# Kernel optimization log

Measured on AMD Instinct MI355X. Metric: run time of the kernel, lower is better.

Reference implementation:

```python
import jax, jax.numpy as jnp
import numpy as np

B, T, I = 32, 128, 512
H, L, O = 512, 2, 512


def _uniform(key, shape, std):
    return jax.random.uniform(key, shape, jnp.float32, -std, std)


def setup_inputs() -> dict:
    key = jax.random.key(0)
    ks = jax.random.split(key, 12)
    std = 1.0 / np.sqrt(H)
    inp = {
        "x": jax.random.normal(ks[0], (B, T, I), jnp.float32),
        # stacked params: [L, 2, ...]; dir 0 = forward cells, dir 1 = reverse cells
        "Wxh": _uniform(ks[1], (L, 2, I, 2 * H), std),
        "bxh": _uniform(ks[2], (L, 2, 2 * H), std),
        "Whh": _uniform(ks[3], (L, 2, H, 2 * H), std),
        "bhh": _uniform(ks[4], (L, 2, 2 * H), std),
        "Wxr": _uniform(ks[5], (L, 2, I, H), std),
        "bxr": _uniform(ks[6], (L, 2, H), std),
        "Whr": _uniform(ks[7], (L, 2, H, H), std),
        "bhr": _uniform(ks[8], (L, 2, H, ), std),
        "Wfc": _uniform(ks[9], (2 * H, O), 1.0 / np.sqrt(2 * H)),
        "bfc": _uniform(ks[10], (O,), 1.0 / np.sqrt(2 * H)),
    }
    return inp


def gru_layer(seq, Wxh_l, bxh_l, Whh_l, bhh_l, Wxr_l, bxr_l, Whr_l, bhr_l):
    # seq: [T, B, I]. Precompute input projections for all timesteps (one big GEMM),
    # then scan the sequential h-dependent part.
    xh = jnp.einsum('tbi,ih->tbh', seq, Wxh_l) + bxh_l  # [T,B,2H]
    xr = jnp.einsum('tbi,ih->tbh', seq, Wxr_l) + bxr_l  # [T,B,H]

    def step(h, inp):
        xh_t, xr_t = inp
        zr = xh_t + h @ Whh_l + bhh_l
        z, r = jnp.split(zr, 2, axis=-1)
        z = jax.nn.sigmoid(z)
        r = jax.nn.sigmoid(r)
        g = jnp.tanh((h @ Whr_l + bhr_l) * r + xr_t)
        h = z * h + (1.0 - z) * g
        return h, h

    h0 = jnp.zeros((seq.shape[1], Whh_l.shape[0]), seq.dtype)
    _, out = jax.lax.scan(step, h0, (xh, xr))
    return out  # [T,B,H]


def reference(x, Wxh, bxh, Whh, bhh, Wxr, bxr, Whr, bhr, Wfc, bfc):
    # Faithful translation of BidirRecurrentModel.forward (GRU mode):
    # forward stream scans time-ordered input; reverse stream independently scans
    # the time-reversed input (the two streams are NOT concatenated between layers).
    seq_f = jnp.transpose(x, (1, 0, 2))   # [T,B,I]
    seq_r = seq_f[::-1]                   # reversed time order
    n_layers = Wxh.shape[0]
    for l in range(n_layers):
        seq_f = gru_layer(seq_f, Wxh[l, 0], bxh[l, 0], Whh[l, 0], bhh[l, 0],
                          Wxr[l, 0], bxr[l, 0], Whr[l, 0], bhr[l, 0])
        seq_r = gru_layer(seq_r, Wxh[l, 1], bxh[l, 1], Whh[l, 1], bhh[l, 1],
                          Wxr[l, 1], bxr[l, 1], Whr[l, 1], bhr[l, 1])
    # out = last fwd timestep; out_rev = FIRST element of reverse-ordered stream
    # (i.e. the reverse cell's state after one step), exactly as in the source.
    out = jnp.concatenate([seq_f[-1], seq_r[0]], axis=1)  # [B, 2H]
    return out @ Wfc + bfc  # [B, O]
```

## Files before the change

### kernel.cpp

```cpp
#include <hip/hip_runtime.h>
#include <hip/hip_bf16.h>

#define PROJ_ELEMS 12582912
#define SEQ_ELEMS  4194304
#define SLAB_PER_BLK 6144

__global__ __launch_bounds__(256)
void proj_kernel(const float* __restrict__ src,
                 const float* __restrict__ Wxh, const float* __restrict__ bxh,
                 const float* __restrict__ Wxr, const float* __restrict__ bxr,
                 __hip_bfloat16* __restrict__ proj, int layer)
{
    __shared__ float As[32][137];
    __shared__ float Ws[32][132];
    const int tid  = threadIdx.x;
    const int col0 = blockIdx.x * 128;
    const int row0 = blockIdx.y * 128;
    const int d    = row0 >> 12;
    const int ld   = layer * 2 + d;
    const int tx = tid & 15, ty = tid >> 4;

    const bool is_xr = (col0 >= 1024);
    const float* Wbase = is_xr ? (Wxr + (size_t)ld * 512 * 512 + (col0 - 1024))
                               : (Wxh + (size_t)ld * 512 * 1024 + col0);
    const int wstride = is_xr ? 512 : 1024;
    const float* bias = is_xr ? (bxr + ld * 512 + (col0 - 1024))
                              : (bxh + ld * 1024 + col0);

    float acc[8][8];
    #pragma unroll
    for (int i = 0; i < 8; i++)
        #pragma unroll
        for (int j = 0; j < 8; j++) acc[i][j] = 0.f;

    for (int k0 = 0; k0 < 512; k0 += 32) {
        #pragma unroll
        for (int v = 0; v < 4; v++) {
            int idx = tid + v * 256;
            int r   = idx >> 3;
            int c4  = (idx & 7) << 2;
            int gm  = row0 + r;
            int rr  = gm & 4095;
            int tt  = rr >> 5, bb = rr & 31;
            const float* p;
            if (layer == 0) {
                int ts = (gm >= 4096) ? (127 - tt) : tt;
                p = src + ((size_t)bb * 128 + ts) * 512 + (k0 + c4);
            } else {
                p = src + (((size_t)(gm >> 12) * 128 + tt) * 32 + bb) * 512 + (k0 + c4);
            }
            float4 vv = *(const float4*)p;
            As[c4 + 0][r] = vv.x; As[c4 + 1][r] = vv.y;
            As[c4 + 2][r] = vv.z; As[c4 + 3][r] = vv.w;
        }
        #pragma unroll
        for (int v = 0; v < 4; v++) {
            int idx = tid + v * 256;
            int kr  = idx >> 5;
            int c4  = (idx & 31) << 2;
            *(float4*)&Ws[kr][c4] = *(const float4*)(Wbase + (size_t)(k0 + kr) * wstride + c4);
        }
        __syncthreads();
        #pragma unroll
        for (int kk = 0; kk < 32; kk++) {
            float a[8], w[8];
            *(float4*)&a[0] = *(const float4*)&As[kk][ty * 8];
            *(float4*)&a[4] = *(const float4*)&As[kk][ty * 8 + 4];
            *(float4*)&w[0] = *(const float4*)&Ws[kk][tx * 8];
            *(float4*)&w[4] = *(const float4*)&Ws[kk][tx * 8 + 4];
            #pragma unroll
            for (int i = 0; i < 8; i++)
                #pragma unroll
                for (int j = 0; j < 8; j++)
                    acc[i][j] += a[i] * w[j];
        }
        __syncthreads();
    }
    #pragma unroll
    for (int i = 0; i < 8; i++) {
        int gm = row0 + ty * 8 + i;
        __hip_bfloat16* dst = proj + (size_t)gm * 1536 + col0 + tx * 8;
        #pragma unroll
        for (int j = 0; j < 8; j++)
            dst[j] = __float2bfloat16(acc[i][j] + bias[tx * 8 + j]);
    }
}

__global__ __launch_bounds__(256)
void repack_kernel(const float* __restrict__ Whh, const float* __restrict__ Whr,
                   float* __restrict__ slabs)
{
    const int blk = blockIdx.x;
    const int ld = blk >> 7, jb = blk & 127;
    const float* WhhL = Whh + (size_t)ld * 512 * 1024;
    const float* WhrL = Whr + (size_t)ld * 512 * 512;
    float* out = slabs + (size_t)blk * SLAB_PER_BLK;
    for (int u = 0; u < 24; u++) {
        int idx = threadIdx.x + u * 256;
        int rec = idx / 12, r3 = idx % 12;
        int g = rec >> 2, cg = rec & 3;
        int e = r3 >> 2, ki = r3 & 3;
        int k = g * 4 + ki, j = jb * 4 + cg;
        float v;
        if (e == 0)      v = WhhL[(size_t)k * 1024 + j];
        else if (e == 1) v = WhhL[(size_t)k * 1024 + 512 + j];
        else             v = WhrL[(size_t)k * 512 + j];
        out[idx] = v;
    }
}

__global__ __launch_bounds__(256)
void step_kernel(const __hip_bfloat16* __restrict__ proj, float* __restrict__ seq,
                 const float* __restrict__ slabs,
                 const float* __restrict__ bhh, const float* __restrict__ bhr,
                 int layer, int t)
{
    __shared__ __align__(16) float hs[32 * 512];
    const int tid = threadIdx.x;
    const int d   = blockIdx.x >> 7;
    const int jb  = blockIdx.x & 127;
    const int ld  = layer * 2 + d;
    const int cg  = tid & 3;
    const int kh  = (tid >> 2) & 1;
    const int b   = tid >> 3;
    const int j   = jb * 4 + cg;
    const int sb  = b & 7;

    float az = 0.f, ar = 0.f, ag = 0.f;
    float hv_self = 0.f;

    if (t > 0) {
        const float* hsrc = seq + ((size_t)(d * 128 + (t - 1)) * 32) * 512;
        #pragma unroll
        for (int v = 0; v < 16; v++) {
            int id = tid + v * 256;
            int bb = id >> 7, g = id & 127;
            float4 hv = *(const float4*)(hsrc + (size_t)id * 4);
            *(float4*)&hs[bb * 512 + ((g ^ (bb & 7)) << 2)] = hv;
        }
        __syncthreads();

        const float4* wrec = (const float4*)slabs + (size_t)(ld * 128 + jb) * 1536;
        #pragma unroll 4
        for (int gg = 0; gg < 64; gg++) {
            int g = kh * 64 + gg;
            float4 h4 = *(const float4*)&hs[b * 512 + ((g ^ sb) << 2)];
            const float4* wp = wrec + (size_t)(g * 4 + cg) * 3;
            float4 wz = wp[0], wr = wp[1], wg = wp[2];
            az += h4.x * wz.x + h4.y * wz.y + h4.z * wz.z + h4.w * wz.w;
            ar += h4.x * wr.x + h4.y * wr.y + h4.z * wr.z + h4.w * wr.w;
            ag += h4.x * wg.x + h4.y * wg.y + h4.z * wg.z + h4.w * wg.w;
        }
        az += __shfl_xor(az, 4, 64);
        ar += __shfl_xor(ar, 4, 64);
        ag += __shfl_xor(ag, 4, 64);
        hv_self = hs[b * 512 + ((jb ^ sb) << 2) + cg];
    }

    const size_t pb = ((size_t)(d * 128 + t) * 32 + b) * 1536;
    float pz = __bfloat162float(proj[pb + j]);
    float pr = __bfloat162float(proj[pb + 512 + j]);
    float pg = __bfloat162float(proj[pb + 1024 + j]);
    float bz = bhh[ld * 1024 + j];
    float br = bhh[ld * 1024 + 512 + j];
    float bg = bhr[ld * 512 + j];
    float z  = 1.f / (1.f + __expf(-(az + pz + bz)));
    float r  = 1.f / (1.f + __expf(-(ar + pr + br)));
    float gt = tanhf((ag + bg) * r + pg);
    float hn = z * hv_self + (1.f - z) * gt;
    if (kh == 0)
        seq[((size_t)(d * 128 + t) * 32 + b) * 512 + j] = hn;
}

__global__ __launch_bounds__(256)
void fc_kernel(const float* __restrict__ seq, const float* __restrict__ Wfc,
               const float* __restrict__ bfc, float* __restrict__ out)
{
    int idx = blockIdx.x * 256 + threadIdx.x;
    int b = idx >> 9, o = idx & 511;
    const float* catf = seq + ((size_t)(0 * 128 + 127) * 32 + b) * 512;
    const float* catr = seq + ((size_t)(1 * 128 + 0) * 32 + b) * 512;
    float acc = bfc[o];
    #pragma unroll 8
    for (int k = 0; k < 512; k++) acc += catf[k] * Wfc[(size_t)k * 512 + o];
    #pragma unroll 8
    for (int k = 0; k < 512; k++) acc += catr[k] * Wfc[(size_t)(512 + k) * 512 + o];
    out[(size_t)b * 512 + o] = acc;
}

extern "C" void kernel_launch(void* const* d_in, const int* in_sizes, int n_in,
                              void* d_out, int out_size, void* d_ws, size_t ws_size,
                              hipStream_t stream) {
    (void)in_sizes; (void)n_in; (void)out_size; (void)ws_size;
    const float* x   = (const float*)d_in[0];
    const float* Wxh = (const float*)d_in[1];
    const float* bxh = (const float*)d_in[2];
    const float* Whh = (const float*)d_in[3];
    const float* bhh = (const float*)d_in[4];
    const float* Wxr = (const float*)d_in[5];
    const float* bxr = (const float*)d_in[6];
    const float* Whr = (const float*)d_in[7];
    const float* bhr = (const float*)d_in[8];
    const float* Wfc = (const float*)d_in[9];
    const float* bfc = (const float*)d_in[10];
    float* out = (float*)d_out;

    char* base = (char*)d_ws;
    __hip_bfloat16* proj = (__hip_bfloat16*)base;
    float* seq   = (float*)(base + (size_t)PROJ_ELEMS * 2);
    float* slabs = seq + SEQ_ELEMS;

    repack_kernel<<<512, 256, 0, stream>>>(Whh, Whr, slabs);

    dim3 pgrid(12, 64);
    proj_kernel<<<pgrid, 256, 0, stream>>>(x, Wxh, bxh, Wxr, bxr, proj, 0);
    for (int t = 0; t < 128; t++)
        step_kernel<<<256, 256, 0, stream>>>(proj, seq, slabs, bhh, bhr, 0, t);
    proj_kernel<<<pgrid, 256, 0, stream>>>(seq, Wxh, bxh, Wxr, bxr, proj, 1);
    for (int t = 0; t < 128; t++)
        step_kernel<<<256, 256, 0, stream>>>(proj, seq, slabs, bhh, bhr, 1, t);
    fc_kernel<<<64, 256, 0, stream>>>(seq, Wfc, bfc, out);
}
```

Before: 2.713 ms.

## Wavefront-pipeline both GRU layers with per-step layer-1 input projection in one launch

Replaces the two sequential 128-step loops (each with its own bulk input projection) with 130 launches of a combined kernel. Each launch runs layer-0 step t, the layer-1 input projection for step t-1, and layer-1 recurrence for step t-2, using ring buffers for intermediate states. This cuts the number of serial launches from 256 plus a projection GEMM to 130, and runs work from different stages concurrently. The cost is a wider grid per launch, a GEMV-style layer-1 projection instead of a tiled GEMM, fp32 intermediate projections for layer 1, and an extra weight repack kernel.

```diff
diff --git a/kernel.cpp b/kernel.cpp
--- a/kernel.cpp
+++ b/kernel.cpp
@@ -1,15 +1,12 @@
 #include <hip/hip_runtime.h>
 #include <hip/hip_bf16.h>
 
-#define PROJ_ELEMS 12582912
-#define SEQ_ELEMS  4194304
-#define SLAB_PER_BLK 6144
 
 __global__ __launch_bounds__(256)
 void proj_kernel(const float* __restrict__ src,
                  const float* __restrict__ Wxh, const float* __restrict__ bxh,
                  const float* __restrict__ Wxr, const float* __restrict__ bxr,
-                 __hip_bfloat16* __restrict__ proj, int layer)
+                 __hip_bfloat16* __restrict__ proj)
 {
     __shared__ float As[32][137];
     __shared__ float Ws[32][132];
@@ -17,7 +14,7 @@
     const int col0 = blockIdx.x * 128;
     const int row0 = blockIdx.y * 128;
     const int d    = row0 >> 12;
-    const int ld   = layer * 2 + d;
+    const int ld   = d;
     const int tx = tid & 15, ty = tid >> 4;
 
     const bool is_xr = (col0 >= 1024);
@@ -42,13 +39,8 @@
             int gm  = row0 + r;
             int rr  = gm & 4095;
             int tt  = rr >> 5, bb = rr & 31;
-            const float* p;
-            if (layer == 0) {
-                int ts = (gm >= 4096) ? (127 - tt) : tt;
-                p = src + ((size_t)bb * 128 + ts) * 512 + (k0 + c4);
-            } else {
-                p = src + (((size_t)(gm >> 12) * 128 + tt) * 32 + bb) * 512 + (k0 + c4);
-            }
+            int ts  = (gm >= 4096) ? (127 - tt) : tt;
+            const float* p = src + ((size_t)bb * 128 + ts) * 512 + (k0 + c4);
             float4 vv = *(const float4*)p;
             As[c4 + 0][r] = vv.x; As[c4 + 1][r] = vv.y;
             As[c4 + 2][r] = vv.z; As[c4 + 3][r] = vv.w;
@@ -94,7 +86,7 @@
     const int ld = blk >> 7, jb = blk & 127;
     const float* WhhL = Whh + (size_t)ld * 512 * 1024;
     const float* WhrL = Whr + (size_t)ld * 512 * 512;
-    float* out = slabs + (size_t)blk * SLAB_PER_BLK;
+    float* out = slabs + (size_t)blk * 6144;
     for (int u = 0; u < 24; u++) {
         int idx = threadIdx.x + u * 256;
         int rec = idx / 12, r3 = idx % 12;
@@ -110,27 +102,35 @@
 }
 
 __global__ __launch_bounds__(256)
-void step_kernel(const __hip_bfloat16* __restrict__ proj, float* __restrict__ seq,
-                 const float* __restrict__ slabs,
-                 const float* __restrict__ bhh, const float* __restrict__ bhr,
-                 int layer, int t)
-{
-    __shared__ __align__(16) float hs[32 * 512];
-    const int tid = threadIdx.x;
-    const int d   = blockIdx.x >> 7;
-    const int jb  = blockIdx.x & 127;
-    const int ld  = layer * 2 + d;
-    const int cg  = tid & 3;
-    const int kh  = (tid >> 2) & 1;
-    const int b   = tid >> 3;
-    const int j   = jb * 4 + cg;
-    const int sb  = b & 7;
-
-    float az = 0.f, ar = 0.f, ag = 0.f;
-    float hv_self = 0.f;
-
-    if (t > 0) {
-        const float* hsrc = seq + ((size_t)(d * 128 + (t - 1)) * 32) * 512;
+void irepack_kernel(const float* __restrict__ Wxh, const float* __restrict__ Wxr,
+                    float* __restrict__ islabs)
+{
+    const int blk = blockIdx.x;
+    const int d = blk >> 7, cb = blk & 127;
+    const float* WxhL = Wxh + (size_t)(2 + d) * 512 * 1024;
+    const float* WxrL = Wxr + (size_t)(2 + d) * 512 * 512;
+    float* out = islabs + (size_t)blk * 6144;
+    for (int u = 0; u < 24; u++) {
+        int idx = threadIdx.x + u * 256;
+        int rec = idx / 12, r3 = idx % 12;
+        int g = rec >> 2, cg = rec & 3;
+        int e = r3 >> 2, ki = r3 & 3;
+        int k = g * 4 + ki, c = cb * 12 + cg * 3 + e;
+        out[idx] = (c < 1024) ? WxhL[(size_t)k * 1024 + c]
+                              : WxrL[(size_t)k * 512 + (c - 1024)];
+    }
+}
+
+template<bool BF16P>
+__device__ __forceinline__ void recur_body(float* hs, int tid, int jb, int ld,
+    const float* hsrc, const float4* wrec, const void* projrow,
+    const float* __restrict__ bhh, const float* __restrict__ bhr,
+    float* out_h, float* out_fc)
+{
+    const int cg = tid & 3, kh = (tid >> 2) & 1, b = tid >> 3, sb = b & 7;
+    const int j = jb * 4 + cg;
+    float az = 0.f, ar = 0.f, ag = 0.f, hv_self = 0.f;
+    if (hsrc) {
         #pragma unroll
         for (int v = 0; v < 16; v++) {
             int id = tid + v * 256;
@@ -139,47 +139,127 @@
             *(float4*)&hs[bb * 512 + ((g ^ (bb & 7)) << 2)] = hv;
         }
         __syncthreads();
-
-        const float4* wrec = (const float4*)slabs + (size_t)(ld * 128 + jb) * 1536;
         #pragma unroll 4
         for (int gg = 0; gg < 64; gg++) {
             int g = kh * 64 + gg;
             float4 h4 = *(const float4*)&hs[b * 512 + ((g ^ sb) << 2)];
             const float4* wp = wrec + (size_t)(g * 4 + cg) * 3;
             float4 wz = wp[0], wr = wp[1], wg = wp[2];
-            az += h4.x * wz.x + h4.y * wz.y + h4.z * wz.z + h4.w * wz.w;
-            ar += h4.x * wr.x + h4.y * wr.y + h4.z * wr.z + h4.w * wr.w;
-            ag += h4.x * wg.x + h4.y * wg.y + h4.z * wg.z + h4.w * wg.w;
+            az += h4.x*wz.x + h4.y*wz.y + h4.z*wz.z + h4.w*wz.w;
+            ar += h4.x*wr.x + h4.y*wr.y + h4.z*wr.z + h4.w*wr.w;
+            ag += h4.x*wg.x + h4.y*wg.y + h4.z*wg.z + h4.w*wg.w;
         }
         az += __shfl_xor(az, 4, 64);
         ar += __shfl_xor(ar, 4, 64);
         ag += __shfl_xor(ag, 4, 64);
         hv_self = hs[b * 512 + ((jb ^ sb) << 2) + cg];
     }
-
-    const size_t pb = ((size_t)(d * 128 + t) * 32 + b) * 1536;
-    float pz = __bfloat162float(proj[pb + j]);
-    float pr = __bfloat162float(proj[pb + 512 + j]);
-    float pg = __bfloat162float(proj[pb + 1024 + j]);
-    float bz = bhh[ld * 1024 + j];
-    float br = bhh[ld * 1024 + 512 + j];
-    float bg = bhr[ld * 512 + j];
-    float z  = 1.f / (1.f + __expf(-(az + pz + bz)));
-    float r  = 1.f / (1.f + __expf(-(ar + pr + br)));
-    float gt = tanhf((ag + bg) * r + pg);
+    float pz, pr, pg;
+    if (BF16P) {
+        const __hip_bfloat16* pp = (const __hip_bfloat16*)projrow + (size_t)b * 1536;
+        pz = __bfloat162float(pp[j]);
+        pr = __bfloat162float(pp[512 + j]);
+        pg = __bfloat162float(pp[1024 + j]);
+    } else {
+        const float* pp = (const float*)projrow + (size_t)b * 1536;
+        pz = pp[j]; pr = pp[512 + j]; pg = pp[1024 + j];
+    }
+    float z  = 1.f / (1.f + __expf(-(az + pz + bhh[ld * 1024 + j])));
+    float r  = 1.f / (1.f + __expf(-(ar + pr + bhh[ld * 1024 + 512 + j])));
+    float gt = tanhf((ag + bhr[ld * 512 + j]) * r + pg);
     float hn = z * hv_self + (1.f - z) * gt;
-    if (kh == 0)
-        seq[((size_t)(d * 128 + t) * 32 + b) * 512 + j] = hn;
-}
-
-__global__ __launch_bounds__(256)
-void fc_kernel(const float* __restrict__ seq, const float* __restrict__ Wfc,
+    if (kh == 0) {
+        out_h[(size_t)b * 512 + j] = hn;
+        if (out_fc) out_fc[(size_t)b * 512 + j] = hn;
+    }
+}
+
+__global__ __launch_bounds__(256)
+void pipe_kernel(const __hip_bfloat16* __restrict__ proj0, float* __restrict__ seq0,
+                 const float* __restrict__ rslabs, const float* __restrict__ islabs,
+                 float* __restrict__ p1, float* __restrict__ h1ring,
+                 float* __restrict__ fcin,
+                 const float* __restrict__ bhh, const float* __restrict__ bhr,
+                 const float* __restrict__ bxh, const float* __restrict__ bxr, int L)
+{
+    __shared__ __align__(16) float hs[32 * 512];
+    const int blk = blockIdx.x, tid = threadIdx.x;
+
+    if (blk < 256) {
+        if (L > 127) return;
+        const int d = blk >> 7, jb = blk & 127, t = L;
+        const float* hsrc = (t == 0) ? nullptr
+                          : seq0 + (size_t)(d * 128 + (t - 1)) * 32 * 512;
+        const float4* wrec = (const float4*)rslabs + (size_t)(d * 128 + jb) * 1536;
+        const void* projrow = proj0 + (size_t)(d * 128 + t) * 32 * 1536;
+        recur_body<true>(hs, tid, jb, d, hsrc, wrec, projrow, bhh, bhr,
+                         seq0 + (size_t)(d * 128 + t) * 32 * 512, nullptr);
+    } else if (blk < 512) {
+        if (L < 2) return;
+        const int t1 = L - 2;
+        const int d = (blk - 256) >> 7, jb = blk & 127;
+        const float* hsrc = (t1 == 0) ? nullptr
+                          : h1ring + (size_t)((((t1 - 1) & 1) * 2) + d) * 32 * 512;
+        const float4* wrec = (const float4*)rslabs + (size_t)((2 + d) * 128 + jb) * 1536;
+        const void* projrow = p1 + (size_t)(((t1 & 1) * 2) + d) * 32 * 1536;
+        float* out_fc = nullptr;
+        if (d == 0 && t1 == 127) out_fc = fcin;
+        if (d == 1 && t1 == 0)   out_fc = fcin + 32 * 512;
+        recur_body<false>(hs, tid, jb, 2 + d, hsrc, wrec, projrow, bhh, bhr,
+                          h1ring + (size_t)(((t1 & 1) * 2) + d) * 32 * 512, out_fc);
+    } else {
+        if (L < 1 || L > 128) return;
+        const int tp = L - 1;
+        const int d = (blk - 512) >> 7, cb = blk & 127;
+        const int cg = tid & 3, kh = (tid >> 2) & 1, b = tid >> 3, sb = b & 7;
+        const float* xsrc = seq0 + (size_t)(d * 128 + tp) * 32 * 512;
+        #pragma unroll
+        for (int v = 0; v < 16; v++) {
+            int id = tid + v * 256;
+            int bb = id >> 7, g = id & 127;
+            float4 hv = *(const float4*)(xsrc + (size_t)id * 4);
+            *(float4*)&hs[bb * 512 + ((g ^ (bb & 7)) << 2)] = hv;
+        }
+        __syncthreads();
+        const float4* wrec = (const float4*)islabs + (size_t)(d * 128 + cb) * 1536;
+        float a0 = 0.f, a1 = 0.f, a2 = 0.f;
+        #pragma unroll 4
+        for (int gg = 0; gg < 64; gg++) {
+            int g = kh * 64 + gg;
+            float4 h4 = *(const float4*)&hs[b * 512 + ((g ^ sb) << 2)];
+            const float4* wp = wrec + (size_t)(g * 4 + cg) * 3;
+            float4 w0 = wp[0], w1 = wp[1], w2 = wp[2];
+            a0 += h4.x*w0.x + h4.y*w0.y + h4.z*w0.z + h4.w*w0.w;
+            a1 += h4.x*w1.x + h4.y*w1.y + h4.z*w1.z + h4.w*w1.w;
+            a2 += h4.x*w2.x + h4.y*w2.y + h4.z*w2.z + h4.w*w2.w;
+        }
+        a0 += __shfl_xor(a0, 4, 64);
+        a1 += __shfl_xor(a1, 4, 64);
+        a2 += __shfl_xor(a2, 4, 64);
+        if (kh == 0) {
+            const int c0 = cb * 12 + cg * 3;
+            float* dst = p1 + (size_t)(((tp & 1) * 2) + d) * 32 * 1536
+                            + (size_t)b * 1536 + c0;
+            float acc[3] = {a0, a1, a2};
+            #pragma unroll
+            for (int e = 0; e < 3; e++) {
+                int c = c0 + e;
+                float bias = (c < 1024) ? bxh[(size_t)(2 + d) * 1024 + c]
+                                        : bxr[(size_t)(2 + d) * 512 + (c - 1024)];
+                dst[e] = acc[e] + bias;
+            }
+        }
+    }
+}
+
+__global__ __launch_bounds__(256)
+void fc_kernel(const float* __restrict__ fcin, const float* __restrict__ Wfc,
                const float* __restrict__ bfc, float* __restrict__ out)
 {
     int idx = blockIdx.x * 256 + threadIdx.x;
     int b = idx >> 9, o = idx & 511;
-    const float* catf = seq + ((size_t)(0 * 128 + 127) * 32 + b) * 512;
-    const float* catr = seq + ((size_t)(1 * 128 + 0) * 32 + b) * 512;
+    const float* catf = fcin + (size_t)b * 512;
+    const float* catr = fcin + 32 * 512 + (size_t)b * 512;
     float acc = bfc[o];
     #pragma unroll 8
     for (int k = 0; k < 512; k++) acc += catf[k] * Wfc[(size_t)k * 512 + o];
@@ -206,18 +286,23 @@
     float* out = (float*)d_out;
 
     char* base = (char*)d_ws;
-    __hip_bfloat16* proj = (__hip_bfloat16*)base;
-    float* seq   = (float*)(base + (size_t)PROJ_ELEMS * 2);
-    float* slabs = seq + SEQ_ELEMS;
-
-    repack_kernel<<<512, 256, 0, stream>>>(Whh, Whr, slabs);
+    __hip_bfloat16* proj0 = (__hip_bfloat16*)base;
+    float* seq0   = (float*)(base + 25165824);
+    float* rslabs = seq0   + 4194304;
+    float* islabs = rslabs + 3145728;
+    float* p1     = islabs + 1572864;
+    float* h1ring = p1     + 196608;
+    float* fcin   = h1ring + 65536;
+
+    repack_kernel<<<512, 256, 0, stream>>>(Whh, Whr, rslabs);
+    irepack_kernel<<<256, 256, 0, stream>>>(Wxh, Wxr, islabs);
 
     dim3 pgrid(12, 64);
-    proj_kernel<<<pgrid, 256, 0, stream>>>(x, Wxh, bxh, Wxr, bxr, proj, 0);
-    for (int t = 0; t < 128; t++)
-        step_kernel<<<256, 256, 0, stream>>>(proj, seq, slabs, bhh, bhr, 0, t);
-    proj_kernel<<<pgrid, 256, 0, stream>>>(seq, Wxh, bxh, Wxr, bxr, proj, 1);
-    for (int t = 0; t < 128; t++)
-        step_kernel<<<256, 256, 0, stream>>>(proj, seq, slabs, bhh, bhr, 1, t);
-    fc_kernel<<<64, 256, 0, stream>>>(seq, Wfc, bfc, out);
-}
+    proj_kernel<<<pgrid, 256, 0, stream>>>(x, Wxh, bxh, Wxr, bxr, proj0);
+
+    for (int L = 0; L < 130; L++)
+        pipe_kernel<<<768, 256, 0, stream>>>(proj0, seq0, rslabs, islabs, p1,
+                                             h1ring, fcin, bhh, bhr, bxh, bxr, L);
+
+    fc_kernel<<<64, 256, 0, stream>>>(fcin, Wfc, bfc, out);
+}
```

Result: slower. 3.214 ms (+18.5%).
